# Kernel tuning notes

Measured on AMD Instinct MI355X. Metric: run time of the kernel, lower is better.

Reference implementation:

```python
import jax, jax.numpy as jnp
import numpy as np

B, Q, P = 4, 512, 512
Q_SIZE, P_SIZE, V_SIZE = 512, 512, 256


def setup_inputs() -> dict:
    key = jax.random.key(0)
    k1, k2, k3, k4, k5 = jax.random.split(key, 5)
    hq = jax.random.normal(k1, (B, Q, Q_SIZE), dtype=jnp.float32)
    hp = jax.random.normal(k2, (B, P, P_SIZE), dtype=jnp.float32)
    # Linear weights stored as [in, out] for x @ W; scaled like default init
    W1 = jax.random.normal(k3, (Q_SIZE, V_SIZE), dtype=jnp.float32) / np.sqrt(Q_SIZE)
    W2 = jax.random.normal(k4, (P_SIZE, V_SIZE), dtype=jnp.float32) / np.sqrt(P_SIZE)
    v = jax.random.normal(k5, (V_SIZE,), dtype=jnp.float32) / np.sqrt(V_SIZE)
    return {"hq": hq, "hp": hp, "W1": W1, "W2": W2, "v": v}


def reference(hq, hp, W1, W2, v):
    # Projections: [B,Q,V], [B,P,V]
    sq = jnp.einsum("bqd,dv->bqv", hq, W1)
    sp = jnp.einsum("bpe,ev->bpv", hp, W2)
    # Additive (Bahdanau) scores: broadcast add -> tanh -> dot with v: [B,P,Q]
    s = jnp.einsum("bpqv,v->bpq", jnp.tanh(sp[:, :, None, :] + sq[:, None, :, :]), v)
    # softmax over Q (dim=2 after squeeze), then weighted sum over hq: [B,P,q_size]
    a = jax.nn.softmax(s, axis=2)
    return jnp.einsum("bpq,bqd->bpd", a, hq)
```

## Files before the change

### kernel.cpp

```cpp
#include <hip/hip_runtime.h>

#define VDIM 256
#define DDIM 512
#define LOG2E     1.4426950408889634f
#define TWO_LOG2E 2.8853900817779268f

typedef float  f32x4   __attribute__((ext_vector_type(4)));
typedef short  short8v __attribute__((ext_vector_type(8)));

__device__ __forceinline__ unsigned short f2bf(float f) {
    unsigned int u = __float_as_uint(f);
    u += 0x7fffu + ((u >> 16) & 1u);
    return (unsigned short)(u >> 16);
}
__device__ __forceinline__ float bf2f(unsigned short b) {
    return __uint_as_float(((unsigned int)b) << 16);
}

__device__ __forceinline__ void split4(const float4 f, uint2* hi, uint2* lo) {
    const unsigned u0 = __float_as_uint(f.x), u1 = __float_as_uint(f.y);
    const unsigned u2 = __float_as_uint(f.z), u3 = __float_as_uint(f.w);
    const unsigned h0 = u0 & 0xFFFF0000u, h1 = u1 & 0xFFFF0000u;
    const unsigned h2 = u2 & 0xFFFF0000u, h3 = u3 & 0xFFFF0000u;
    hi->x = (u0 >> 16) | h1;
    hi->y = (u2 >> 16) | h3;
    const float l0 = f.x - __uint_as_float(h0), l1 = f.y - __uint_as_float(h1);
    const float l2 = f.z - __uint_as_float(h2), l3 = f.w - __uint_as_float(h3);
    lo->x = (__float_as_uint(l0) >> 16) | (__float_as_uint(l1) & 0xFFFF0000u);
    lo->y = (__float_as_uint(l2) >> 16) | (__float_as_uint(l3) & 0xFFFF0000u);
}

__global__ __launch_bounds__(256) void w_transpose(
    const float* __restrict__ W1, const float* __restrict__ W2,
    ushort* __restrict__ W1T_hi, ushort* __restrict__ W1T_lo,
    ushort* __restrict__ W2T_hi, ushort* __restrict__ W2T_lo)
{
    const float* src = blockIdx.z ? W2 : W1;
    ushort* dhi = blockIdx.z ? W2T_hi : W1T_hi;
    ushort* dlo = blockIdx.z ? W2T_lo : W1T_lo;
    const int r0 = blockIdx.y << 6, c0 = blockIdx.x << 6;

    __shared__ float tile[64][65];
    const int t = threadIdx.x;
    #pragma unroll
    for (int i = 0; i < 4; ++i) {
        const int r = (i << 4) + (t >> 4);
        const int c = (t & 15) << 2;
        const float4 v = *(const float4*)(src + (size_t)(r0 + r) * 256 + c0 + c);
        tile[r][c + 0] = v.x; tile[r][c + 1] = v.y;
        tile[r][c + 2] = v.z; tile[r][c + 3] = v.w;
    }
    __syncthreads();
    #pragma unroll
    for (int i = 0; i < 4; ++i) {
        const int a  = (i << 4) + (t >> 4);
        const int bb = (t & 15) << 2;
        ushort4 hi, lo;
        float f;
        f = tile[bb + 0][a]; hi.x = f2bf(f); lo.x = f2bf(f - bf2f(hi.x));
        f = tile[bb + 1][a]; hi.y = f2bf(f); lo.y = f2bf(f - bf2f(hi.y));
        f = tile[bb + 2][a]; hi.z = f2bf(f); lo.z = f2bf(f - bf2f(hi.z));
        f = tile[bb + 3][a]; hi.w = f2bf(f); lo.w = f2bf(f - bf2f(hi.w));
        const size_t o = (size_t)(c0 + a) * 512 + r0 + bb;
        *(ushort4*)(dhi + o) = hi;
        *(ushort4*)(dlo + o) = lo;
    }
}

#define SWZ(r, c) (((r) << 8) + ((c) ^ (((r) & 15) << 4)))

__global__ __launch_bounds__(256) void proj_and_transpose(
    const float* __restrict__ hq, const float* __restrict__ hp,
    const ushort* __restrict__ W1T_hi, const ushort* __restrict__ W1T_lo,
    const ushort* __restrict__ W2T_hi, const ushort* __restrict__ W2T_lo,
    ushort* __restrict__ hqT_hi, ushort* __restrict__ hqT_lo,
    float* __restrict__ EqT, float* __restrict__ Ep)
{
    __shared__ __attribute__((aligned(16))) char smem[32768];
    const int bid = blockIdx.x;
    const int t = threadIdx.x;

    if (bid >= 256) {
        const int k  = bid - 256;
        const int z  = k >> 6;
        const int r0 = ((k >> 3) & 7) << 6, c0 = (k & 7) << 6;
        const float* src = hq + ((size_t)z << 18);
        ushort* dhi = hqT_hi + ((size_t)z << 18);
        ushort* dlo = hqT_lo + ((size_t)z << 18);
        float (*tile)[65] = (float(*)[65])smem;
        #pragma unroll
        for (int i = 0; i < 4; ++i) {
            const int r = (i << 4) + (t >> 4);
            const int c = (t & 15) << 2;
            const float4 v = *(const float4*)(src + (size_t)(r0 + r) * 512 + c0 + c);
            tile[r][c + 0] = v.x; tile[r][c + 1] = v.y;
            tile[r][c + 2] = v.z; tile[r][c + 3] = v.w;
        }
        __syncthreads();
        #pragma unroll
        for (int i = 0; i < 4; ++i) {
            const int a  = (i << 4) + (t >> 4);
            const int bb = (t & 15) << 2;
            ushort4 hi, lo;
            float f;
            f = tile[bb + 0][a]; hi.x = f2bf(f); lo.x = f2bf(f - bf2f(hi.x));
            f = tile[bb + 1][a]; hi.y = f2bf(f); lo.y = f2bf(f - bf2f(hi.y));
            f = tile[bb + 2][a]; hi.z = f2bf(f); lo.z = f2bf(f - bf2f(hi.z));
            f = tile[bb + 3][a]; hi.w = f2bf(f); lo.w = f2bf(f - bf2f(hi.w));
            const size_t o = (size_t)(c0 + a) * 512 + r0 + bb;
            *(ushort4*)(dhi + o) = hi;
            *(ushort4*)(dlo + o) = lo;
        }
        return;
    }

    const int by = bid >> 2;
    const bool isQ = by < 32;
    const int m0 = (by & 31) << 6;
    const int n0 = (bid & 3) << 6;
    const float*  __restrict__ A   = isQ ? hq : hp;
    const ushort* __restrict__ Bhi = isQ ? W1T_hi : W2T_hi;
    const ushort* __restrict__ Blo = isQ ? W1T_lo : W2T_lo;

    char* AsB = smem;
    char* BsB = smem + 16384;

    const int w = t >> 6, l = t & 63;
    const int moff = (w & 1) << 5, noff = (w >> 1) << 5;

    f32x4 acc[2][2];
    #pragma unroll
    for (int i = 0; i < 2; ++i)
        #pragma unroll
        for (int j = 0; j < 2; ++j)
            acc[i][j] = (f32x4){0.f, 0.f, 0.f, 0.f};

    const int sr = t >> 2;
    const int sc = t & 3;
    const size_t argA = (size_t)(m0 + sr) * 512;
    const size_t argB = (size_t)(n0 + sr) * 512;

    for (int k0 = 0; k0 < 512; k0 += 64) {
        const float4 f0 = *(const float4*)(A + argA + k0 + (sc << 4) + 0);
        const float4 f1 = *(const float4*)(A + argA + k0 + (sc << 4) + 4);
        const float4 f2 = *(const float4*)(A + argA + k0 + (sc << 4) + 8);
        const float4 f3 = *(const float4*)(A + argA + k0 + (sc << 4) + 12);
        const uint4 b0 = *(const uint4*)(Bhi + argB + k0 + (sc << 4));
        const uint4 b1 = *(const uint4*)(Bhi + argB + k0 + (sc << 4) + 8);
        const uint4 b2 = *(const uint4*)(Blo + argB + k0 + (sc << 4));
        const uint4 b3 = *(const uint4*)(Blo + argB + k0 + (sc << 4) + 8);

        uint4 ah0, al0, ah1, al1;
        split4(f0, (uint2*)&ah0.x, (uint2*)&al0.x);
        split4(f1, (uint2*)&ah0.z, (uint2*)&al0.z);
        split4(f2, (uint2*)&ah1.x, (uint2*)&al1.x);
        split4(f3, (uint2*)&ah1.z, (uint2*)&al1.z);

        __syncthreads();
        *(uint4*)(AsB + SWZ(sr, (sc << 5)))            = ah0;
        *(uint4*)(AsB + SWZ(sr, (sc << 5) + 16))       = ah1;
        *(uint4*)(AsB + SWZ(sr, 128 + (sc << 5)))      = al0;
        *(uint4*)(AsB + SWZ(sr, 128 + (sc << 5) + 16)) = al1;
        *(uint4*)(BsB + SWZ(sr, (sc << 5)))            = b0;
        *(uint4*)(BsB + SWZ(sr, (sc << 5) + 16))       = b1;
        *(uint4*)(BsB + SWZ(sr, 128 + (sc << 5)))      = b2;
        *(uint4*)(BsB + SWZ(sr, 128 + (sc << 5) + 16)) = b3;
        __syncthreads();

        #pragma unroll
        for (int kc = 0; kc < 2; ++kc) {
            const int colh = (kc << 6) + ((l >> 4) << 4);
            short8v ahi[2], alo[2], bhi[2], blo[2];
            #pragma unroll
            for (int mt = 0; mt < 2; ++mt) {
                const int r = moff + (mt << 4) + (l & 15);
                ahi[mt] = *(const short8v*)(AsB + SWZ(r, colh));
                alo[mt] = *(const short8v*)(AsB + SWZ(r, colh + 128));
            }
            #pragma unroll
            for (int nt = 0; nt < 2; ++nt) {
                const int r = noff + (nt << 4) + (l & 15);
                bhi[nt] = *(const short8v*)(BsB + SWZ(r, colh));
                blo[nt] = *(const short8v*)(BsB + SWZ(r, colh + 128));
            }
            #pragma unroll
            for (int mt = 0; mt < 2; ++mt)
                #pragma unroll
                for (int nt = 0; nt < 2; ++nt) {
                    acc[mt][nt] = __builtin_amdgcn_mfma_f32_16x16x32_bf16(ahi[mt], bhi[nt], acc[mt][nt], 0, 0, 0);
                    acc[mt][nt] = __builtin_amdgcn_mfma_f32_16x16x32_bf16(ahi[mt], blo[nt], acc[mt][nt], 0, 0, 0);
                    acc[mt][nt] = __builtin_amdgcn_mfma_f32_16x16x32_bf16(alo[mt], bhi[nt], acc[mt][nt], 0, 0, 0);
                }
        }
    }

    #pragma unroll
    for (int mt = 0; mt < 2; ++mt)
        #pragma unroll
        for (int nt = 0; nt < 2; ++nt)
            #pragma unroll
            for (int r = 0; r < 4; ++r) {
                const int row = m0 + moff + (mt << 4) + ((l >> 4) << 2) + r;
                const int col = n0 + noff + (nt << 4) + (l & 15);
                const float e = __builtin_amdgcn_exp2f(acc[mt][nt][r] * TWO_LOG2E);
                if (isQ) {
                    const int bb = row >> 9, q = row & 511;
                    EqT[((((size_t)bb << 6) + (col >> 2)) * 512 + q) * 4 + (col & 3)] = e;
                } else {
                    Ep[(size_t)row * VDIM + col] = e;
                }
            }
}

__global__ __launch_bounds__(256) void out_mfma(
    const ushort* __restrict__ Ahi, const ushort* __restrict__ Alo,
    const ushort* __restrict__ Bhi_, const ushort* __restrict__ Blo_,
    float* __restrict__ C)
{
    const int m0 = blockIdx.y << 6;
    const int n0 = blockIdx.x << 6;
    const size_t off = (size_t)(m0 >> 9) << 18;
    const ushort* __restrict__ Bhi = Bhi_ + off;
    const ushort* __restrict__ Blo = Blo_ + off;

    __shared__ __attribute__((aligned(16))) ushort As[64 * 128];
    __shared__ __attribute__((aligned(16))) ushort Bs[64 * 128];
    char* AsB = (char*)As;
    char* BsB = (char*)Bs;

    const int t = threadIdx.x;
    const int w = t >> 6, l = t & 63;
    const int moff = (w & 1) << 5, noff = (w >> 1) << 5;

    f32x4 acc[2][2];
    #pragma unroll
    for (int i = 0; i < 2; ++i)
        #pragma unroll
        for (int j = 0; j < 2; ++j)
            acc[i][j] = (f32x4){0.f, 0.f, 0.f, 0.f};

    const int sr = t >> 2;
    const int sc = t & 3;
    const size_t argA = (size_t)(m0 + sr) * 512;
    const size_t argB = (size_t)(n0 + sr) * 512;

    for (int k0 = 0; k0 < 512; k0 += 64) {
        const uint4 a0 = *(const uint4*)(Ahi + argA + k0 + (sc << 4));
        const uint4 a1 = *(const uint4*)(Ahi + argA + k0 + (sc << 4) + 8);
        const uint4 a2 = *(const uint4*)(Alo + argA + k0 + (sc << 4));
        const uint4 a3 = *(const uint4*)(Alo + argA + k0 + (sc << 4) + 8);
        const uint4 b0 = *(const uint4*)(Bhi + argB + k0 + (sc << 4));
        const uint4 b1 = *(const uint4*)(Bhi + argB + k0 + (sc << 4) + 8);
        const uint4 b2 = *(const uint4*)(Blo + argB + k0 + (sc << 4));
        const uint4 b3 = *(const uint4*)(Blo + argB + k0 + (sc << 4) + 8);
        __syncthreads();
        *(uint4*)(AsB + SWZ(sr, (sc << 5)))            = a0;
        *(uint4*)(AsB + SWZ(sr, (sc << 5) + 16))       = a1;
        *(uint4*)(AsB + SWZ(sr, 128 + (sc << 5)))      = a2;
        *(uint4*)(AsB + SWZ(sr, 128 + (sc << 5) + 16)) = a3;
        *(uint4*)(BsB + SWZ(sr, (sc << 5)))            = b0;
        *(uint4*)(BsB + SWZ(sr, (sc << 5) + 16))       = b1;
        *(uint4*)(BsB + SWZ(sr, 128 + (sc << 5)))      = b2;
        *(uint4*)(BsB + SWZ(sr, 128 + (sc << 5) + 16)) = b3;
        __syncthreads();
        #pragma unroll
        for (int kc = 0; kc < 2; ++kc) {
            const int colh = (kc << 6) + ((l >> 4) << 4);
            short8v ahi[2], alo[2], bhi[2], blo[2];
            #pragma unroll
            for (int mt = 0; mt < 2; ++mt) {
                const int r = moff + (mt << 4) + (l & 15);
                ahi[mt] = *(const short8v*)(AsB + SWZ(r, colh));
                alo[mt] = *(const short8v*)(AsB + SWZ(r, colh + 128));
            }
            #pragma unroll
            for (int nt = 0; nt < 2; ++nt) {
                const int r = noff + (nt << 4) + (l & 15);
                bhi[nt] = *(const short8v*)(BsB + SWZ(r, colh));
                blo[nt] = *(const short8v*)(BsB + SWZ(r, colh + 128));
            }
            #pragma unroll
            for (int mt = 0; mt < 2; ++mt)
                #pragma unroll
                for (int nt = 0; nt < 2; ++nt) {
                    acc[mt][nt] = __builtin_amdgcn_mfma_f32_16x16x32_bf16(ahi[mt], bhi[nt], acc[mt][nt], 0, 0, 0);
                    acc[mt][nt] = __builtin_amdgcn_mfma_f32_16x16x32_bf16(ahi[mt], blo[nt], acc[mt][nt], 0, 0, 0);
                    acc[mt][nt] = __builtin_amdgcn_mfma_f32_16x16x32_bf16(alo[mt], bhi[nt], acc[mt][nt], 0, 0, 0);
                }
        }
    }

    #pragma unroll
    for (int mt = 0; mt < 2; ++mt)
        #pragma unroll
        for (int nt = 0; nt < 2; ++nt)
            #pragma unroll
            for (int r = 0; r < 4; ++r) {
                const int row = m0 + moff + (mt << 4) + ((l >> 4) << 2) + r;
                const int col = n0 + noff + (nt << 4) + (l & 15);
                C[(size_t)row * 512 + col] = acc[mt][nt][r];
            }
}

template<bool FUSED>
__global__ __launch_bounds__(512) void score_softmax(
    const float4* __restrict__ EqT, const float* __restrict__ Ep,
    const float* __restrict__ vvec, const float* __restrict__ hq,
    ushort* __restrict__ a_hi, ushort* __restrict__ a_lo,
    float* __restrict__ out)
{
    const int blk = blockIdx.x;
    const int b   = blk >> 7;
    const int p0  = (blk & 127) << 2;

    __shared__ __attribute__((aligned(16))) float score[4][512];
    const int t = threadIdx.x;

    const float4* __restrict__ wv = (const float4*)vvec;
    const float4* __restrict__ eqp = EqT + ((size_t)b << 15) + t;
    const float*  epb              = Ep + (size_t)((b << 9) + p0) * VDIM;

    float a0 = 0.f, a1 = 0.f, a2 = 0.f, a3 = 0.f;
    float4 e = eqp[0];

    #pragma unroll 4
    for (int vi = 0; vi < 64; ++vi) {
        const float4 ec = e;
        if (vi < 63) e = eqp[(vi + 1) << 9];
        const float4 w = wv[vi];
#define ROWTERM(i, accv) { \
        const float4 p = *((const float4*)(epb + (i) * VDIM) + vi); \
        const float t0 = fmaf(p.x, ec.x, 1.f), t1 = fmaf(p.y, ec.y, 1.f); \
        const float t2 = fmaf(p.z, ec.z, 1.f), t3 = fmaf(p.w, ec.w, 1.f); \
        const float d01 = t0 * t1, d23 = t2 * t3, den = d01 * d23; \
        const float n01 = fmaf(w.x, t1, w.y * t0); \
        const float n23 = fmaf(w.z, t3, w.w * t2); \
        const float num = fmaf(n01, d23, n23 * d01); \
        accv = fmaf(num, __builtin_amdgcn_rcpf(den), accv); }
        ROWTERM(0, a0) ROWTERM(1, a1) ROWTERM(2, a2) ROWTERM(3, a3)
#undef ROWTERM
    }
    score[0][t] = a0; score[1][t] = a1; score[2][t] = a2; score[3][t] = a3;
    __syncthreads();

    {
        const int wid = t >> 6, lane = t & 63;
        if (wid < 4) {
            float vals[8];
            float m = -1e30f;
            #pragma unroll
            for (int i = 0; i < 8; ++i) {
                vals[i] = -2.f * score[wid][lane + (i << 6)];
                m = fmaxf(m, vals[i]);
            }
            #pragma unroll
            for (int off = 32; off; off >>= 1) m = fmaxf(m, __shfl_xor(m, off));
            float sum = 0.f;
            #pragma unroll
            for (int i = 0; i < 8; ++i) {
                vals[i] = __builtin_amdgcn_exp2f((vals[i] - m) * LOG2E);
                sum += vals[i];
            }
            #pragma unroll
            for (int off = 32; off; off >>= 1) sum += __shfl_xor(sum, off);
            const float inv = __builtin_amdgcn_rcpf(sum);
            #pragma unroll
            for (int i = 0; i < 8; ++i) score[wid][lane + (i << 6)] = vals[i] * inv;
        }
    }
    __syncthreads();

    if (!FUSED) {
        #pragma unroll
        for (int r = 0; r < 4; ++r) {
            const float f = score[r][t];
            const ushort h  = f2bf(f);
            const ushort lo = f2bf(f - bf2f(h));
            a_hi[(size_t)((b << 9) + p0 + r) * 512 + t] = h;
            a_lo[(size_t)((b << 9) + p0 + r) * 512 + t] = lo;
        }
    } else {
        float ax[4] = {};
        #pragma unroll 4
        for (int q = 0; q < 512; ++q) {
            const float h = hq[(size_t)((b << 9) + q) * DDIM + t];
            #pragma unroll
            for (int r = 0; r < 4; ++r) ax[r] = fmaf(score[r][q], h, ax[r]);
        }
        #pragma unroll
        for (int r = 0; r < 4; ++r)
            out[(size_t)((b << 9) + p0 + r) * DDIM + t] = ax[r];
    }
}

__global__ __launch_bounds__(256) void proj_exp_gemm_f32(
    const float* __restrict__ hq, const float* __restrict__ hp,
    const float* __restrict__ W1, const float* __restrict__ W2,
    float* __restrict__ Eq, float* __restrict__ Ep)
{
    const int by = blockIdx.y;
    const float *A, *W;
    if (by < 64) { A = hq; W = W1; }
    else         { A = hp; W = W2; }
    const int m0 = (by & 63) * 32;
    const int n0 = blockIdx.x * 64;

    __shared__ __attribute__((aligned(16))) float As[16][36];
    __shared__ __attribute__((aligned(16))) float Bs[16][68];

    const int tid  = threadIdx.x;
    const int tr = tid >> 4, tc = tid & 15;
    const int la_r = tid >> 3, la_c = (tid & 7) << 1;
    const int lb_r = tid >> 4, lb_c = (tid & 15) << 2;

    float acc[2][4] = {};
    for (int k0 = 0; k0 < 512; k0 += 16) {
        float2 a2 = *(const float2*)(A + (size_t)(m0 + la_r) * 512 + k0 + la_c);
        float4 b4 = *(const float4*)(W + (size_t)(k0 + lb_r) * VDIM + n0 + lb_c);
        __syncthreads();
        As[la_c + 0][la_r] = a2.x;
        As[la_c + 1][la_r] = a2.y;
        *(float4*)&Bs[lb_r][lb_c] = b4;
        __syncthreads();
        #pragma unroll
        for (int kk = 0; kk < 16; ++kk) {
            float2 av = *(const float2*)&As[kk][tr << 1];
            float4 bv = *(const float4*)&Bs[kk][tc << 2];
            const float* ap = (const float*)&av;
            const float* bp = (const float*)&bv;
            #pragma unroll
            for (int i = 0; i < 2; ++i)
                #pragma unroll
                for (int j = 0; j < 4; ++j)
                    acc[i][j] = fmaf(ap[i], bp[j], acc[i][j]);
        }
    }
    if (by < 64) {
        float4* EqT = (float4*)Eq;
        const int bb = m0 >> 9, qb = m0 & 511;
        const int vi = (blockIdx.x << 4) + tc;
        #pragma unroll
        for (int i = 0; i < 2; ++i) {
            float4 r;
            r.x = __builtin_amdgcn_exp2f(acc[i][0] * TWO_LOG2E);
            r.y = __builtin_amdgcn_exp2f(acc[i][1] * TWO_LOG2E);
            r.z = __builtin_amdgcn_exp2f(acc[i][2] * TWO_LOG2E);
            r.w = __builtin_amdgcn_exp2f(acc[i][3] * TWO_LOG2E);
            EqT[((size_t)(bb << 6) + vi) * 512 + qb + (tr << 1) + i] = r;
        }
    } else {
        #pragma unroll
        for (int i = 0; i < 2; ++i) {
            float4 r;
            r.x = __builtin_amdgcn_exp2f(acc[i][0] * TWO_LOG2E);
            r.y = __builtin_amdgcn_exp2f(acc[i][1] * TWO_LOG2E);
            r.z = __builtin_amdgcn_exp2f(acc[i][2] * TWO_LOG2E);
            r.w = __builtin_amdgcn_exp2f(acc[i][3] * TWO_LOG2E);
            *(float4*)(Ep + (size_t)(m0 + (tr << 1) + i) * VDIM + n0 + (tc << 2)) = r;
        }
    }
}

extern "C" void kernel_launch(void* const* d_in, const int* in_sizes, int n_in,
                              void* d_out, int out_size, void* d_ws, size_t ws_size,
                              hipStream_t stream)
{
    const float* hq = (const float*)d_in[0];
    const float* hp = (const float*)d_in[1];
    const float* W1 = (const float*)d_in[2];
    const float* W2 = (const float*)d_in[3];
    const float* vv = (const float*)d_in[4];
    float* out = (float*)d_out;

    float* EqT = (float*)d_ws;
    float* Ep  = EqT + 524288;
    ushort* u  = (ushort*)(Ep + 524288);
    ushort* hqT_hi = u; u += 1048576;
    ushort* hqT_lo = u; u += 1048576;
    ushort* W1T_hi = u; u += 131072;
    ushort* W1T_lo = u; u += 131072;
    ushort* W2T_hi = u; u += 131072;
    ushort* W2T_lo = u; u += 131072;
    ushort* a_hi   = u; u += 1048576;
    ushort* a_lo   = u; u += 1048576;
    const size_t need = (size_t)((char*)u - (char*)d_ws);

    if (ws_size >= need) {
        w_transpose<<<dim3(4, 8, 2), 256, 0, stream>>>(
            W1, W2, W1T_hi, W1T_lo, W2T_hi, W2T_lo);
        proj_and_transpose<<<512, 256, 0, stream>>>(
            hq, hp, W1T_hi, W1T_lo, W2T_hi, W2T_lo, hqT_hi, hqT_lo, EqT, Ep);
        score_softmax<false><<<512, 512, 0, stream>>>(
            (const float4*)EqT, Ep, vv, hq, a_hi, a_lo, out);
        out_mfma<<<dim3(8, 32), 256, 0, stream>>>(a_hi, a_lo, hqT_hi, hqT_lo, out);
    } else {
        proj_exp_gemm_f32<<<dim3(4, 128), 256, 0, stream>>>(hq, hp, W1, W2, EqT, Ep);
        score_softmax<true><<<512, 512, 0, stream>>>(
            (const float4*)EqT, Ep, vv, hq, nullptr, nullptr, out);
    }
}
```

Before: 58.53 us.

## Score 8 P-rows per block with split-V threads; halve out_mfma M-tile

Adds a new score kernel in which each 1024-thread block covers 8 P rows and splits the V dimension across two thread halves, combining the partial sums in shared memory before the softmax. Each loaded Eq value is now reused across 8 rows instead of 4, which cuts EqT global traffic per score. The output MFMA GEMM tile shrinks from 64 to 32 rows, doubling its grid to 512 blocks for better CU occupancy at the cost of less operand reuse. The fallback path is split into its own kernel, and the explicit Eq prefetch is dropped.

```diff
diff --git a/kernel.cpp b/kernel.cpp
--- a/kernel.cpp
+++ b/kernel.cpp
@@ -212,101 +212,231 @@
             }
 }
 
+__global__ __launch_bounds__(1024) void score_softmax8(
+    const float4* __restrict__ EqT, const float* __restrict__ Ep,
+    const float* __restrict__ vvec,
+    ushort* __restrict__ a_hi, ushort* __restrict__ a_lo)
+{
+    const int blk = blockIdx.x;
+    const int b   = blk >> 6;
+    const int p0  = (blk & 63) << 3;
+
+    __shared__ __attribute__((aligned(16))) float part[8][1024];
+    const int t  = threadIdx.x;
+    const int q  = t & 511;
+    const int vh = t >> 9;
+
+    const float4* __restrict__ wv  = (const float4*)vvec;
+    const float4* __restrict__ eqp = EqT + ((size_t)b << 15) + ((size_t)vh << 14) + q;
+    const float*  epb              = Ep + (size_t)((b << 9) + p0) * VDIM;
+
+    float a0 = 0.f, a1 = 0.f, a2 = 0.f, a3 = 0.f;
+    float a4 = 0.f, a5 = 0.f, a6 = 0.f, a7 = 0.f;
+
+    #pragma unroll 4
+    for (int vi = 0; vi < 32; ++vi) {
+        const float4 e = eqp[vi << 9];
+        const int vg = (vh << 5) + vi;
+        const float4 w = wv[vg];
+#define ROWTERM(i, accv) { \
+        const float4 p = *((const float4*)(epb + (i) * VDIM) + vg); \
+        const float t0 = fmaf(p.x, e.x, 1.f), t1 = fmaf(p.y, e.y, 1.f); \
+        const float t2 = fmaf(p.z, e.z, 1.f), t3 = fmaf(p.w, e.w, 1.f); \
+        const float d01 = t0 * t1, d23 = t2 * t3, den = d01 * d23; \
+        const float n01 = fmaf(w.x, t1, w.y * t0); \
+        const float n23 = fmaf(w.z, t3, w.w * t2); \
+        const float num = fmaf(n01, d23, n23 * d01); \
+        accv = fmaf(num, __builtin_amdgcn_rcpf(den), accv); }
+        ROWTERM(0, a0) ROWTERM(1, a1) ROWTERM(2, a2) ROWTERM(3, a3)
+        ROWTERM(4, a4) ROWTERM(5, a5) ROWTERM(6, a6) ROWTERM(7, a7)
+#undef ROWTERM
+    }
+    part[0][t] = a0; part[1][t] = a1; part[2][t] = a2; part[3][t] = a3;
+    part[4][t] = a4; part[5][t] = a5; part[6][t] = a6; part[7][t] = a7;
+    __syncthreads();
+
+    {
+        const int wid = t >> 6, lane = t & 63;
+        if (wid < 8) {
+            float vals[8];
+            float m = -1e30f;
+            #pragma unroll
+            for (int i = 0; i < 8; ++i) {
+                const int qq = lane + (i << 6);
+                vals[i] = -2.f * (part[wid][qq] + part[wid][qq + 512]);
+                m = fmaxf(m, vals[i]);
+            }
+            #pragma unroll
+            for (int off = 32; off; off >>= 1) m = fmaxf(m, __shfl_xor(m, off));
+            float sum = 0.f;
+            #pragma unroll
+            for (int i = 0; i < 8; ++i) {
+                vals[i] = __builtin_amdgcn_exp2f((vals[i] - m) * LOG2E);
+                sum += vals[i];
+            }
+            #pragma unroll
+            for (int off = 32; off; off >>= 1) sum += __shfl_xor(sum, off);
+            const float inv = __builtin_amdgcn_rcpf(sum);
+            #pragma unroll
+            for (int i = 0; i < 8; ++i) part[wid][lane + (i << 6)] = vals[i] * inv;
+        }
+    }
+    __syncthreads();
+
+    #pragma unroll
+    for (int r = 0; r < 4; ++r) {
+        const int row = (vh << 2) + r;
+        const float f = part[row][q];
+        const ushort h  = f2bf(f);
+        const ushort lo = f2bf(f - bf2f(h));
+        a_hi[(size_t)((b << 9) + p0 + row) * 512 + q] = h;
+        a_lo[(size_t)((b << 9) + p0 + row) * 512 + q] = lo;
+    }
+}
+
 __global__ __launch_bounds__(256) void out_mfma(
     const ushort* __restrict__ Ahi, const ushort* __restrict__ Alo,
     const ushort* __restrict__ Bhi_, const ushort* __restrict__ Blo_,
     float* __restrict__ C)
 {
-    const int m0 = blockIdx.y << 6;
+    const int m0 = blockIdx.y << 5;
     const int n0 = blockIdx.x << 6;
     const size_t off = (size_t)(m0 >> 9) << 18;
     const ushort* __restrict__ Bhi = Bhi_ + off;
     const ushort* __restrict__ Blo = Blo_ + off;
 
-    __shared__ __attribute__((aligned(16))) ushort As[64 * 128];
+    __shared__ __attribute__((aligned(16))) ushort As[32 * 128];
     __shared__ __attribute__((aligned(16))) ushort Bs[64 * 128];
     char* AsB = (char*)As;
     char* BsB = (char*)Bs;
 
     const int t = threadIdx.x;
     const int w = t >> 6, l = t & 63;
-    const int moff = (w & 1) << 5, noff = (w >> 1) << 5;
-
-    f32x4 acc[2][2];
-    #pragma unroll
-    for (int i = 0; i < 2; ++i)
-        #pragma unroll
-        for (int j = 0; j < 2; ++j)
-            acc[i][j] = (f32x4){0.f, 0.f, 0.f, 0.f};
-
-    const int sr = t >> 2;
-    const int sc = t & 3;
-    const size_t argA = (size_t)(m0 + sr) * 512;
-    const size_t argB = (size_t)(n0 + sr) * 512;
+    const int moff = (w & 1) << 4, noff = (w >> 1) << 5;
+
+    f32x4 acc[2];
+    acc[0] = (f32x4){0.f, 0.f, 0.f, 0.f};
+    acc[1] = (f32x4){0.f, 0.f, 0.f, 0.f};
+
+    const int sra = t >> 3, sca = t & 7;
+    const int srb = t >> 2, scb = t & 3;
+    const size_t argA = (size_t)(m0 + sra) * 512;
+    const size_t argB = (size_t)(n0 + srb) * 512;
 
     for (int k0 = 0; k0 < 512; k0 += 64) {
-        const uint4 a0 = *(const uint4*)(Ahi + argA + k0 + (sc << 4));
-        const uint4 a1 = *(const uint4*)(Ahi + argA + k0 + (sc << 4) + 8);
-        const uint4 a2 = *(const uint4*)(Alo + argA + k0 + (sc << 4));
-        const uint4 a3 = *(const uint4*)(Alo + argA + k0 + (sc << 4) + 8);
-        const uint4 b0 = *(const uint4*)(Bhi + argB + k0 + (sc << 4));
-        const uint4 b1 = *(const uint4*)(Bhi + argB + k0 + (sc << 4) + 8);
-        const uint4 b2 = *(const uint4*)(Blo + argB + k0 + (sc << 4));
-        const uint4 b3 = *(const uint4*)(Blo + argB + k0 + (sc << 4) + 8);
-        __syncthreads();
-        *(uint4*)(AsB + SWZ(sr, (sc << 5)))            = a0;
-        *(uint4*)(AsB + SWZ(sr, (sc << 5) + 16))       = a1;
-        *(uint4*)(AsB + SWZ(sr, 128 + (sc << 5)))      = a2;
-        *(uint4*)(AsB + SWZ(sr, 128 + (sc << 5) + 16)) = a3;
-        *(uint4*)(BsB + SWZ(sr, (sc << 5)))            = b0;
-        *(uint4*)(BsB + SWZ(sr, (sc << 5) + 16))       = b1;
-        *(uint4*)(BsB + SWZ(sr, 128 + (sc << 5)))      = b2;
-        *(uint4*)(BsB + SWZ(sr, 128 + (sc << 5) + 16)) = b3;
+        const uint4 a0 = *(const uint4*)(Ahi + argA + k0 + (sca << 3));
+        const uint4 a1 = *(const uint4*)(Alo + argA + k0 + (sca << 3));
+        const uint4 b0 = *(const uint4*)(Bhi + argB + k0 + (scb << 4));
+        const uint4 b1 = *(const uint4*)(Bhi + argB + k0 + (scb << 4) + 8);
+        const uint4 b2 = *(const uint4*)(Blo + argB + k0 + (scb << 4));
+        const uint4 b3 = *(const uint4*)(Blo + argB + k0 + (scb << 4) + 8);
+        __syncthreads();
+        *(uint4*)(AsB + SWZ(sra, (sca << 4)))          = a0;
+        *(uint4*)(AsB + SWZ(sra, 128 + (sca << 4)))    = a1;
+        *(uint4*)(BsB + SWZ(srb, (scb << 5)))          = b0;
+        *(uint4*)(BsB + SWZ(srb, (scb << 5) + 16))     = b1;
+        *(uint4*)(BsB + SWZ(srb, 128 + (scb << 5)))    = b2;
+        *(uint4*)(BsB + SWZ(srb, 128 + (scb << 5) + 16)) = b3;
         __syncthreads();
         #pragma unroll
         for (int kc = 0; kc < 2; ++kc) {
             const int colh = (kc << 6) + ((l >> 4) << 4);
-            short8v ahi[2], alo[2], bhi[2], blo[2];
-            #pragma unroll
-            for (int mt = 0; mt < 2; ++mt) {
-                const int r = moff + (mt << 4) + (l & 15);
-                ahi[mt] = *(const short8v*)(AsB + SWZ(r, colh));
-                alo[mt] = *(const short8v*)(AsB + SWZ(r, colh + 128));
-            }
+            const int ra = moff + (l & 15);
+            const short8v ahi = *(const short8v*)(AsB + SWZ(ra, colh));
+            const short8v alo = *(const short8v*)(AsB + SWZ(ra, colh + 128));
             #pragma unroll
             for (int nt = 0; nt < 2; ++nt) {
-                const int r = noff + (nt << 4) + (l & 15);
-                bhi[nt] = *(const short8v*)(BsB + SWZ(r, colh));
-                blo[nt] = *(const short8v*)(BsB + SWZ(r, colh + 128));
-            }
-            #pragma unroll
-            for (int mt = 0; mt < 2; ++mt)
+                const int rb = noff + (nt << 4) + (l & 15);
+                const short8v bhi = *(const short8v*)(BsB + SWZ(rb, colh));
+                const short8v blo = *(const short8v*)(BsB + SWZ(rb, colh + 128));
+                acc[nt] = __builtin_amdgcn_mfma_f32_16x16x32_bf16(ahi, bhi, acc[nt], 0, 0, 0);
+                acc[nt] = __builtin_amdgcn_mfma_f32_16x16x32_bf16(ahi, blo, acc[nt], 0, 0, 0);
+                acc[nt] = __builtin_amdgcn_mfma_f32_16x16x32_bf16(alo, bhi, acc[nt], 0, 0, 0);
+            }
+        }
+    }
+
+    #pragma unroll
+    for (int nt = 0; nt < 2; ++nt)
+        #pragma unroll
+        for (int r = 0; r < 4; ++r) {
+            const int row = m0 + moff + ((l >> 4) << 2) + r;
+            const int col = n0 + noff + (nt << 4) + (l & 15);
+            C[(size_t)row * 512 + col] = acc[nt][r];
+        }
+}
+
+__global__ __launch_bounds__(256) void proj_exp_gemm_f32(
+    const float* __restrict__ hq, const float* __restrict__ hp,
+    const float* __restrict__ W1, const float* __restrict__ W2,
+    float* __restrict__ Eq, float* __restrict__ Ep)
+{
+    const int by = blockIdx.y;
+    const float *A, *W;
+    if (by < 64) { A = hq; W = W1; }
+    else         { A = hp; W = W2; }
+    const int m0 = (by & 63) * 32;
+    const int n0 = blockIdx.x * 64;
+
+    __shared__ __attribute__((aligned(16))) float As[16][36];
+    __shared__ __attribute__((aligned(16))) float Bs[16][68];
+
+    const int tid  = threadIdx.x;
+    const int tr = tid >> 4, tc = tid & 15;
+    const int la_r = tid >> 3, la_c = (tid & 7) << 1;
+    const int lb_r = tid >> 4, lb_c = (tid & 15) << 2;
+
+    float acc[2][4] = {};
+    for (int k0 = 0; k0 < 512; k0 += 16) {
+        float2 a2 = *(const float2*)(A + (size_t)(m0 + la_r) * 512 + k0 + la_c);
+        float4 b4 = *(const float4*)(W + (size_t)(k0 + lb_r) * VDIM + n0 + lb_c);
+        __syncthreads();
+        As[la_c + 0][la_r] = a2.x;
+        As[la_c + 1][la_r] = a2.y;
+        *(float4*)&Bs[lb_r][lb_c] = b4;
+        __syncthreads();
+        #pragma unroll
+        for (int kk = 0; kk < 16; ++kk) {
+            float2 av = *(const float2*)&As[kk][tr << 1];
+            float4 bv = *(const float4*)&Bs[kk][tc << 2];
+            const float* ap = (const float*)&av;
+            const float* bp = (const float*)&bv;
+            #pragma unroll
+            for (int i = 0; i < 2; ++i)
                 #pragma unroll
-                for (int nt = 0; nt < 2; ++nt) {
-                    acc[mt][nt] = __builtin_amdgcn_mfma_f32_16x16x32_bf16(ahi[mt], bhi[nt], acc[mt][nt], 0, 0, 0);
-                    acc[mt][nt] = __builtin_amdgcn_mfma_f32_16x16x32_bf16(ahi[mt], blo[nt], acc[mt][nt], 0, 0, 0);
-                    acc[mt][nt] = __builtin_amdgcn_mfma_f32_16x16x32_bf16(alo[mt], bhi[nt], acc[mt][nt], 0, 0, 0);
-                }
-        }
-    }
-
-    #pragma unroll
-    for (int mt = 0; mt < 2; ++mt)
-        #pragma unroll
-        for (int nt = 0; nt < 2; ++nt)
-            #pragma unroll
-            for (int r = 0; r < 4; ++r) {
-                const int row = m0 + moff + (mt << 4) + ((l >> 4) << 2) + r;
-                const int col = n0 + noff + (nt << 4) + (l & 15);
-                C[(size_t)row * 512 + col] = acc[mt][nt][r];
-            }
-}
-
-template<bool FUSED>
-__global__ __launch_bounds__(512) void score_softmax(
+                for (int j = 0; j < 4; ++j)
+                    acc[i][j] = fmaf(ap[i], bp[j], acc[i][j]);
+        }
+    }
+    if (by < 64) {
+        float4* EqT = (float4*)Eq;
+        const int bb = m0 >> 9, qb = m0 & 511;
+        const int vi = (blockIdx.x << 4) + tc;
+        #pragma unroll
+        for (int i = 0; i < 2; ++i) {
+            float4 r;
+            r.x = __builtin_amdgcn_exp2f(acc[i][0] * TWO_LOG2E);
+            r.y = __builtin_amdgcn_exp2f(acc[i][1] * TWO_LOG2E);
+            r.z = __builtin_amdgcn_exp2f(acc[i][2] * TWO_LOG2E);
+            r.w = __builtin_amdgcn_exp2f(acc[i][3] * TWO_LOG2E);
+            EqT[((size_t)(bb << 6) + vi) * 512 + qb + (tr << 1) + i] = r;
+        }
+    } else {
+        #pragma unroll
+        for (int i = 0; i < 2; ++i) {
+            float4 r;
+            r.x = __builtin_amdgcn_exp2f(acc[i][0] * TWO_LOG2E);
+            r.y = __builtin_amdgcn_exp2f(acc[i][1] * TWO_LOG2E);
+            r.z = __builtin_amdgcn_exp2f(acc[i][2] * TWO_LOG2E);
+            r.w = __builtin_amdgcn_exp2f(acc[i][3] * TWO_LOG2E);
+            *(float4*)(Ep + (size_t)(m0 + (tr << 1) + i) * VDIM + n0 + (tc << 2)) = r;
+        }
+    }
+}
+
+__global__ __launch_bounds__(512) void score_fused(
     const float4* __restrict__ EqT, const float* __restrict__ Ep,
     const float* __restrict__ vvec, const float* __restrict__ hq,
-    ushort* __restrict__ a_hi, ushort* __restrict__ a_lo,
     float* __restrict__ out)
 {
     const int blk = blockIdx.x;
@@ -316,22 +446,19 @@
     __shared__ __attribute__((aligned(16))) float score[4][512];
     const int t = threadIdx.x;
 
-    const float4* __restrict__ wv = (const float4*)vvec;
+    const float4* __restrict__ wv  = (const float4*)vvec;
     const float4* __restrict__ eqp = EqT + ((size_t)b << 15) + t;
     const float*  epb              = Ep + (size_t)((b << 9) + p0) * VDIM;
 
     float a0 = 0.f, a1 = 0.f, a2 = 0.f, a3 = 0.f;
-    float4 e = eqp[0];
-
     #pragma unroll 4
     for (int vi = 0; vi < 64; ++vi) {
-        const float4 ec = e;
-        if (vi < 63) e = eqp[(vi + 1) << 9];
+        const float4 e = eqp[vi << 9];
         const float4 w = wv[vi];
 #define ROWTERM(i, accv) { \
         const float4 p = *((const float4*)(epb + (i) * VDIM) + vi); \
-        const float t0 = fmaf(p.x, ec.x, 1.f), t1 = fmaf(p.y, ec.y, 1.f); \
-        const float t2 = fmaf(p.z, ec.z, 1.f), t3 = fmaf(p.w, ec.w, 1.f); \
+        const float t0 = fmaf(p.x, e.x, 1.f), t1 = fmaf(p.y, e.y, 1.f); \
+        const float t2 = fmaf(p.z, e.z, 1.f), t3 = fmaf(p.w, e.w, 1.f); \
         const float d01 = t0 * t1, d23 = t2 * t3, den = d01 * d23; \
         const float n01 = fmaf(w.x, t1, w.y * t0); \
         const float n23 = fmaf(w.z, t3, w.w * t2); \
@@ -342,7 +469,6 @@
     }
     score[0][t] = a0; score[1][t] = a1; score[2][t] = a2; score[3][t] = a3;
     __syncthreads();
-
     {
         const int wid = t >> 6, lane = t & 63;
         if (wid < 4) {
@@ -369,96 +495,16 @@
         }
     }
     __syncthreads();
-
-    if (!FUSED) {
-        #pragma unroll
-        for (int r = 0; r < 4; ++r) {
-            const float f = score[r][t];
-            const ushort h  = f2bf(f);
-            const ushort lo = f2bf(f - bf2f(h));
-            a_hi[(size_t)((b << 9) + p0 + r) * 512 + t] = h;
-            a_lo[(size_t)((b << 9) + p0 + r) * 512 + t] = lo;
-        }
-    } else {
-        float ax[4] = {};
-        #pragma unroll 4
-        for (int q = 0; q < 512; ++q) {
-            const float h = hq[(size_t)((b << 9) + q) * DDIM + t];
-            #pragma unroll
-            for (int r = 0; r < 4; ++r) ax[r] = fmaf(score[r][q], h, ax[r]);
-        }
-        #pragma unroll
-        for (int r = 0; r < 4; ++r)
-            out[(size_t)((b << 9) + p0 + r) * DDIM + t] = ax[r];
-    }
-}
-
-__global__ __launch_bounds__(256) void proj_exp_gemm_f32(
-    const float* __restrict__ hq, const float* __restrict__ hp,
-    const float* __restrict__ W1, const float* __restrict__ W2,
-    float* __restrict__ Eq, float* __restrict__ Ep)
-{
-    const int by = blockIdx.y;
-    const float *A, *W;
-    if (by < 64) { A = hq; W = W1; }
-    else         { A = hp; W = W2; }
-    const int m0 = (by & 63) * 32;
-    const int n0 = blockIdx.x * 64;
-
-    __shared__ __attribute__((aligned(16))) float As[16][36];
-    __shared__ __attribute__((aligned(16))) float Bs[16][68];
-
-    const int tid  = threadIdx.x;
-    const int tr = tid >> 4, tc = tid & 15;
-    const int la_r = tid >> 3, la_c = (tid & 7) << 1;
-    const int lb_r = tid >> 4, lb_c = (tid & 15) << 2;
-
-    float acc[2][4] = {};
-    for (int k0 = 0; k0 < 512; k0 += 16) {
-        float2 a2 = *(const float2*)(A + (size_t)(m0 + la_r) * 512 + k0 + la_c);
-        float4 b4 = *(const float4*)(W + (size_t)(k0 + lb_r) * VDIM + n0 + lb_c);
-        __syncthreads();
-        As[la_c + 0][la_r] = a2.x;
-        As[la_c + 1][la_r] = a2.y;
-        *(float4*)&Bs[lb_r][lb_c] = b4;
-        __syncthreads();
-        #pragma unroll
-        for (int kk = 0; kk < 16; ++kk) {
-            float2 av = *(const float2*)&As[kk][tr << 1];
-            float4 bv = *(const float4*)&Bs[kk][tc << 2];
-            const float* ap = (const float*)&av;
-            const float* bp = (const float*)&bv;
-            #pragma unroll
-            for (int i = 0; i < 2; ++i)
-                #pragma unroll
-                for (int j = 0; j < 4; ++j)
-                    acc[i][j] = fmaf(ap[i], bp[j], acc[i][j]);
-        }
-    }
-    if (by < 64) {
-        float4* EqT = (float4*)Eq;
-        const int bb = m0 >> 9, qb = m0 & 511;
-        const int vi = (blockIdx.x << 4) + tc;
-        #pragma unroll
-        for (int i = 0; i < 2; ++i) {
-            float4 r;
-            r.x = __builtin_amdgcn_exp2f(acc[i][0] * TWO_LOG2E);
-            r.y = __builtin_amdgcn_exp2f(acc[i][1] * TWO_LOG2E);
-            r.z = __builtin_amdgcn_exp2f(acc[i][2] * TWO_LOG2E);
-            r.w = __builtin_amdgcn_exp2f(acc[i][3] * TWO_LOG2E);
-            EqT[((size_t)(bb << 6) + vi) * 512 + qb + (tr << 1) + i] = r;
-        }
-    } else {
-        #pragma unroll
-        for (int i = 0; i < 2; ++i) {
-            float4 r;
-            r.x = __builtin_amdgcn_exp2f(acc[i][0] * TWO_LOG2E);
-            r.y = __builtin_amdgcn_exp2f(acc[i][1] * TWO_LOG2E);
-            r.z = __builtin_amdgcn_exp2f(acc[i][2] * TWO_LOG2E);
-            r.w = __builtin_amdgcn_exp2f(acc[i][3] * TWO_LOG2E);
-            *(float4*)(Ep + (size_t)(m0 + (tr << 1) + i) * VDIM + n0 + (tc << 2)) = r;
-        }
-    }
+    float ax[4] = {};
+    #pragma unroll 4
+    for (int q = 0; q < 512; ++q) {
+        const float h = hq[(size_t)((b << 9) + q) * DDIM + t];
+        #pragma unroll
+        for (int r = 0; r < 4; ++r) ax[r] = fmaf(score[r][q], h, ax[r]);
+    }
+    #pragma unroll
+    for (int r = 0; r < 4; ++r)
+        out[(size_t)((b << 9) + p0 + r) * DDIM + t] = ax[r];
 }
 
 extern "C" void kernel_launch(void* const* d_in, const int* in_sizes, int n_in,
@@ -490,12 +536,12 @@
             W1, W2, W1T_hi, W1T_lo, W2T_hi, W2T_lo);
         proj_and_transpose<<<512, 256, 0, stream>>>(
             hq, hp, W1T_hi, W1T_lo, W2T_hi, W2T_lo, hqT_hi, hqT_lo, EqT, Ep);
-        score_softmax<false><<<512, 512, 0, stream>>>(
-            (const float4*)EqT, Ep, vv, hq, a_hi, a_lo, out);
-        out_mfma<<<dim3(8, 32), 256, 0, stream>>>(a_hi, a_lo, hqT_hi, hqT_lo, out);
+        score_softmax8<<<256, 1024, 0, stream>>>(
+            (const float4*)EqT, Ep, vv, a_hi, a_lo);
+        out_mfma<<<dim3(8, 64), 256, 0, stream>>>(a_hi, a_lo, hqT_hi, hqT_lo, out);
     } else {
         proj_exp_gemm_f32<<<dim3(4, 128), 256, 0, stream>>>(hq, hp, W1, W2, EqT, Ep);
-        score_softmax<true><<<512, 512, 0, stream>>>(
-            (const float4*)EqT, Ep, vv, hq, nullptr, nullptr, out);
-    }
-}
+        score_fused<<<512, 512, 0, stream>>>(
+            (const float4*)EqT, Ep, vv, hq, out);
+    }
+}
```

Result: slower. 113.0 us (+93.1%).
